# Kernel optimization log

Measured on AMD Instinct MI355X. Metric: run time of the kernel, lower is better.

Reference implementation:

```python
import jax, jax.numpy as jnp
import numpy as np

N = 100000      # nodes
NE = 1250000    # edges
D = 64          # in_dim == out_dim
H = 8           # heads
DH = D // H     # per-head dim


def setup_inputs() -> dict:
    key = jax.random.key(0)
    ks = jax.random.split(key, 7)
    s = 1.0 / np.sqrt(D)
    return {
        "x": jax.random.normal(ks[0], (N, D), jnp.float32),
        "edge_attr": jax.random.normal(ks[1], (NE, D), jnp.float32),
        "WQ": jax.random.normal(ks[2], (D, D), jnp.float32) * s,
        "WK": jax.random.normal(ks[3], (D, D), jnp.float32) * s,
        "WV": jax.random.normal(ks[4], (D, D), jnp.float32) * s,
        "WE": jax.random.normal(ks[5], (D, D), jnp.float32) * s,
        "edge_index": jax.random.randint(ks[6], (2, NE), 0, N, dtype=jnp.int32),
    }


def reference(x, edge_attr, WQ, WK, WV, WE, edge_index):
    # Linear projections (torch Linear y = x W^T; here W is stored [in,out])
    Q = (x @ WQ).reshape(N, H, DH)
    K = (x @ WK).reshape(N, H, DH)
    V = (x @ WV).reshape(N, H, DH)
    Ef = (edge_attr @ WE).reshape(NE, H, DH)

    src = edge_index[0]
    dst = edge_index[1]

    # per-edge score: exp(clamp(sum_d K[src]*Q[dst]*E / sqrt(DH), -5, 5))
    score = (K[src] * Q[dst]) * (1.0 / np.sqrt(DH)) * Ef  # [E,H,DH]
    score = jnp.exp(jnp.clip(score.sum(-1, keepdims=True), -5.0, 5.0))  # [E,H,1]

    msg = V[src] * score  # [E,H,DH]
    wV = jax.ops.segment_sum(msg, dst, num_segments=N)    # [N,H,DH]
    Z = jax.ops.segment_sum(score, dst, num_segments=N)   # [N,H,1]

    h_out = wV / (Z + 1e-6)
    return h_out.reshape(N, H * DH)
```

## Files before the change

kernel.cpp:

```cpp
#include <hip/hip_runtime.h>
#include <hip/hip_bf16.h>

#define NN    100000
#define NEDGE 1250000

typedef __attribute__((ext_vector_type(8))) short bf16x8;
typedef __attribute__((ext_vector_type(8))) unsigned short u16x8;
typedef __attribute__((ext_vector_type(4))) float f32x4;

__device__ __forceinline__ short f2bf(float f) {
    unsigned u = __float_as_uint(f);
    u += 0x7FFFu + ((u >> 16) & 1u);
    return (short)(u >> 16);
}
__device__ __forceinline__ float bf2f(unsigned short u) {
    return __uint_as_float(((unsigned)u) << 16);
}

constexpr size_t OFF_Q    = 0;
constexpr size_t OFF_KB   = OFF_Q    + (size_t)NN * 64 * 4;
constexpr size_t OFF_VB   = OFF_KB   + (size_t)NN * 64 * 2;
constexpr size_t OFF_SRT  = OFF_VB   + (size_t)NN * 64 * 2;
constexpr size_t OFF_HIST = OFF_SRT  + (size_t)NEDGE * 8;
constexpr size_t OFF_EX   = OFF_HIST + (size_t)NN * 4;
constexpr size_t OFF_BSUM = OFF_EX   + (size_t)NN * 4;
constexpr size_t OFF_BOFF = OFF_BSUM + 512 * 4;
constexpr size_t OFF_START= OFF_BOFF + 512 * 4;
constexpr size_t OFF_CUR  = OFF_START+ (size_t)(NN + 1) * 4;
constexpr size_t WS_NEED  = OFF_CUR  + (size_t)NN * 4;
constexpr int NB_SCAN = (NN + 255) / 256;

__global__ __launch_bounds__(256) void qkv_kernel(
    const float* __restrict__ x,
    const float* __restrict__ WQ, const float* __restrict__ WK,
    const float* __restrict__ WV,
    float* __restrict__ Qf, unsigned short* __restrict__ Kb,
    unsigned short* __restrict__ Vb)
{
    const int lane = threadIdx.x & 63;
    const int wid  = threadIdx.x >> 6;
    const int gw   = blockIdx.x * 4 + wid;
    const int nw   = gridDim.x * 4;
    const int colb = lane & 15;
    const int krow = (lane >> 4) * 8;

    bf16x8 Bf[3][4][2];
    const float* Ws[3] = {WQ, WK, WV};
    #pragma unroll
    for (int m = 0; m < 3; ++m)
        #pragma unroll
        for (int n = 0; n < 4; ++n)
            #pragma unroll
            for (int kh = 0; kh < 2; ++kh) {
                bf16x8 b;
                #pragma unroll
                for (int j = 0; j < 8; ++j)
                    b[j] = f2bf(Ws[m][(size_t)(kh * 32 + krow + j) * 64 + n * 16 + colb]);
                Bf[m][n][kh] = b;
            }

    for (int tile = gw; tile < NN / 16; tile += nw) {
        const int r0 = tile * 16;
        const float* xr = x + (size_t)(r0 + colb) * 64 + krow;
        f32x4 a0 = *(const f32x4*)(xr);
        f32x4 a1 = *(const f32x4*)(xr + 4);
        f32x4 a2 = *(const f32x4*)(xr + 32);
        f32x4 a3 = *(const f32x4*)(xr + 36);
        bf16x8 Alo, Ahi;
        #pragma unroll
        for (int j = 0; j < 4; ++j) {
            Alo[j]     = f2bf(a0[j]);
            Alo[4 + j] = f2bf(a1[j]);
            Ahi[j]     = f2bf(a2[j]);
            Ahi[4 + j] = f2bf(a3[j]);
        }
        #pragma unroll
        for (int m = 0; m < 3; ++m) {
            #pragma unroll
            for (int n = 0; n < 4; ++n) {
                f32x4 acc = {0.f, 0.f, 0.f, 0.f};
                acc = __builtin_amdgcn_mfma_f32_16x16x32_bf16(Alo, Bf[m][n][0], acc, 0, 0, 0);
                acc = __builtin_amdgcn_mfma_f32_16x16x32_bf16(Ahi, Bf[m][n][1], acc, 0, 0, 0);
                #pragma unroll
                for (int q = 0; q < 4; ++q) {
                    const size_t idx = (size_t)(r0 + (lane >> 4) * 4 + q) * 64 + n * 16 + colb;
                    if (m == 0)      Qf[idx] = acc[q];
                    else if (m == 1) Kb[idx] = (unsigned short)f2bf(acc[q]);
                    else             Vb[idx] = (unsigned short)f2bf(acc[q]);
                }
            }
        }
    }
}

__global__ void zero_hist_kernel(int* __restrict__ hist) {
    const int i = blockIdx.x * blockDim.x + threadIdx.x;
    if (i < NN) hist[i] = 0;
}

__global__ void hist_kernel(const int* __restrict__ ei, int* __restrict__ hist) {
    const int e = blockIdx.x * blockDim.x + threadIdx.x;
    if (e < NEDGE) atomicAdd(&hist[ei[NEDGE + e]], 1);
}

__global__ __launch_bounds__(256) void scanA_kernel(
    const int* __restrict__ hist, int* __restrict__ ex, int* __restrict__ bsum)
{
    __shared__ int wsum[4];
    const int i = blockIdx.x * 256 + threadIdx.x;
    const int lane = threadIdx.x & 63, wid = threadIdx.x >> 6;
    const int v = (i < NN) ? hist[i] : 0;
    int incl = v;
    #pragma unroll
    for (int off = 1; off < 64; off <<= 1) {
        int t = __shfl_up(incl, off);
        if (lane >= off) incl += t;
    }
    if (lane == 63) wsum[wid] = incl;
    __syncthreads();
    int pre = 0, bt = 0;
    #pragma unroll
    for (int w = 0; w < 4; ++w) { int s = wsum[w]; bt += s; if (w < wid) pre += s; }
    if (i < NN) ex[i] = incl - v + pre;
    if (threadIdx.x == 0) bsum[blockIdx.x] = bt;
}

__global__ __launch_bounds__(512) void scanB_kernel(
    const int* __restrict__ bsum, int* __restrict__ boff)
{
    __shared__ int wsum[8];
    const int i = threadIdx.x;
    const int lane = i & 63, wid = i >> 6;
    const int v = (i < NB_SCAN) ? bsum[i] : 0;
    int incl = v;
    #pragma unroll
    for (int off = 1; off < 64; off <<= 1) {
        int t = __shfl_up(incl, off);
        if (lane >= off) incl += t;
    }
    if (lane == 63) wsum[wid] = incl;
    __syncthreads();
    int pre = 0;
    #pragma unroll
    for (int w = 0; w < 8; ++w) { if (w < wid) pre += wsum[w]; }
    if (i < NB_SCAN) boff[i] = incl - v + pre;
}

__global__ void scanC_kernel(const int* __restrict__ ex, const int* __restrict__ boff,
                             int* __restrict__ start, int* __restrict__ cursor)
{
    const int i = blockIdx.x * blockDim.x + threadIdx.x;
    if (i < NN) {
        const int s = ex[i] + boff[i >> 8];
        start[i] = s;
        cursor[i] = s;
    } else if (i == NN) {
        start[NN] = NEDGE;
    }
}

__global__ void scatter_kernel(const int* __restrict__ ei, int* __restrict__ cursor,
                               int2* __restrict__ sorted)
{
    const int e = blockIdx.x * blockDim.x + threadIdx.x;
    if (e < NEDGE) {
        const int dst = ei[NEDGE + e];
        const int pos = atomicAdd(&cursor[dst], 1);
        sorted[pos] = make_int2(ei[e], e);
    }
}

__global__ __launch_bounds__(256) void agg_kernel(
    const float* __restrict__ Qn, const unsigned short* __restrict__ Kb,
    const unsigned short* __restrict__ Vb,
    const float* __restrict__ edge_attr, const float* __restrict__ WE,
    const int* __restrict__ start, const int2* __restrict__ sorted,
    float* __restrict__ out)
{
    const int lane = threadIdx.x & 63;
    const int wid  = threadIdx.x >> 6;
    const int gw   = (blockIdx.x * blockDim.x + threadIdx.x) >> 6;
    const int nw   = (gridDim.x * blockDim.x) >> 6;
    const int colb = lane & 15;
    const int krow = (lane >> 4) * 8;
    const int el   = lane >> 3;
    const int h    = lane & 7;
    const float c  = 0.35355339059327373f;

    __shared__ float efs_all[4][16][68];
    __shared__ int   srcs_all[4][16];
    float (*efs)[68] = efs_all[wid];
    int*   srcs      = srcs_all[wid];

    bf16x8 Bf[4][2];
    #pragma unroll
    for (int n = 0; n < 4; ++n)
        #pragma unroll
        for (int kh = 0; kh < 2; ++kh) {
            bf16x8 b;
            #pragma unroll
            for (int j = 0; j < 8; ++j)
                b[j] = f2bf(WE[(size_t)(kh * 32 + krow + j) * 64 + n * 16 + colb]);
            Bf[n][kh] = b;
        }

    for (int dst = gw; dst < NN; dst += nw) {
        const int beg = start[dst], end = start[dst + 1];
        if (beg == end) {
            if (el == 0) {
                float* op = out + (size_t)dst * 64 + h * 8;
                const f32x4 zz = {0.f, 0.f, 0.f, 0.f};
                *(f32x4*)(op)     = zz;
                *(f32x4*)(op + 4) = zz;
            }
            continue;
        }
        const float* qp = Qn + (size_t)dst * 64 + h * 8;
        const f32x4 q0 = *(const f32x4*)(qp);
        const f32x4 q1 = *(const f32x4*)(qp + 4);
        f32x4 av0 = {0.f, 0.f, 0.f, 0.f};
        f32x4 av1 = {0.f, 0.f, 0.f, 0.f};
        float az = 0.f;

        for (int j = beg; j < end; j += 16) {
            int rpos = j + colb;
            if (rpos >= end) rpos = beg;
            const int2 se = sorted[rpos];
            if (lane < 16) srcs[lane] = se.x;
            const float* ear = edge_attr + (size_t)se.y * 64 + krow;
            f32x4 a0 = *(const f32x4*)(ear);
            f32x4 a1 = *(const f32x4*)(ear + 4);
            f32x4 a2 = *(const f32x4*)(ear + 32);
            f32x4 a3 = *(const f32x4*)(ear + 36);
            bf16x8 Alo, Ahi;
            #pragma unroll
            for (int jj = 0; jj < 4; ++jj) {
                Alo[jj]     = f2bf(a0[jj]);
                Alo[4 + jj] = f2bf(a1[jj]);
                Ahi[jj]     = f2bf(a2[jj]);
                Ahi[4 + jj] = f2bf(a3[jj]);
            }
            const int rbase = (lane >> 4) * 4;
            #pragma unroll
            for (int n = 0; n < 4; ++n) {
                f32x4 z = {0.f, 0.f, 0.f, 0.f};
                z = __builtin_amdgcn_mfma_f32_16x16x32_bf16(Alo, Bf[n][0], z, 0, 0, 0);
                z = __builtin_amdgcn_mfma_f32_16x16x32_bf16(Ahi, Bf[n][1], z, 0, 0, 0);
                #pragma unroll
                for (int q = 0; q < 4; ++q)
                    efs[rbase + q][n * 16 + colb] = z[q];
            }
            asm volatile("s_waitcnt lgkmcnt(0)" ::: "memory");
            __builtin_amdgcn_sched_barrier(0);

            #pragma unroll
            for (int t = 0; t < 2; ++t) {
                const int er  = el + t * 8;
                const bool act = (j + er) < end;
                const int srcT = srcs[er];
                const u16x8 kT = *(const u16x8*)(Kb + (size_t)srcT * 64 + h * 8);
                const u16x8 vT = *(const u16x8*)(Vb + (size_t)srcT * 64 + h * 8);
                const f32x4 e0 = *(const f32x4*)(&efs[er][h * 8]);
                const f32x4 e1 = *(const f32x4*)(&efs[er][h * 8 + 4]);
                float tt = 0.f;
                #pragma unroll
                for (int d = 0; d < 4; ++d) {
                    tt += bf2f(kT[d])     * q0[d] * e0[d];
                    tt += bf2f(kT[4 + d]) * q1[d] * e1[d];
                }
                const float sc = act ? __expf(fminf(fmaxf(tt * c, -5.f), 5.f)) : 0.f;
                az += sc;
                #pragma unroll
                for (int d = 0; d < 4; ++d) {
                    av0[d] += bf2f(vT[d])     * sc;
                    av1[d] += bf2f(vT[4 + d]) * sc;
                }
            }
        }

        #pragma unroll
        for (int off = 8; off < 64; off <<= 1) {
            az += __shfl_xor(az, off);
            #pragma unroll
            for (int d = 0; d < 4; ++d) {
                av0[d] += __shfl_xor(av0[d], off);
                av1[d] += __shfl_xor(av1[d], off);
            }
        }

        if (el == 0) {
            const float inv = 1.f / (az + 1e-6f);
            f32x4 o0, o1;
            #pragma unroll
            for (int d = 0; d < 4; ++d) { o0[d] = av0[d] * inv; o1[d] = av1[d] * inv; }
            float* op = out + (size_t)dst * 64 + h * 8;
            *(f32x4*)(op)     = o0;
            *(f32x4*)(op + 4) = o1;
        }
    }
}

__global__ __launch_bounds__(256) void edge_kernel_fb(
    const float* __restrict__ edge_attr, const float* __restrict__ WE,
    const float* __restrict__ Qn, const unsigned short* __restrict__ Kb,
    const unsigned short* __restrict__ Vb, const int* __restrict__ ei,
    float* __restrict__ outAcc, float* __restrict__ Z)
{
    const int lane = threadIdx.x & 63;
    const int wid  = threadIdx.x >> 6;
    const int gw   = blockIdx.x * 4 + wid;
    const int nw   = gridDim.x * 4;
    const int colb = lane & 15;
    const int krow = (lane >> 4) * 8;
    const int b8   = (lane >> 3) & 1;

    bf16x8 Bf[4][2];
    #pragma unroll
    for (int n = 0; n < 4; ++n)
        #pragma unroll
        for (int kh = 0; kh < 2; ++kh) {
            bf16x8 b;
            #pragma unroll
            for (int j = 0; j < 8; ++j)
                b[j] = f2bf(WE[(size_t)(kh * 32 + krow + j) * 64 + n * 16 + colb]);
            Bf[n][kh] = b;
        }

    const float inv_sqrt_dh = 0.35355339059327373f;

    for (int tile = gw; tile < NEDGE / 16; tile += nw) {
        const int e0 = tile * 16;
        const float* ear = edge_attr + (size_t)(e0 + colb) * 64 + krow;
        f32x4 a0 = *(const f32x4*)(ear);
        f32x4 a1 = *(const f32x4*)(ear + 4);
        f32x4 a2 = *(const f32x4*)(ear + 32);
        f32x4 a3 = *(const f32x4*)(ear + 36);
        bf16x8 Alo, Ahi;
        #pragma unroll
        for (int j = 0; j < 4; ++j) {
            Alo[j]     = f2bf(a0[j]);
            Alo[4 + j] = f2bf(a1[j]);
            Ahi[j]     = f2bf(a2[j]);
            Ahi[4 + j] = f2bf(a3[j]);
        }
        f32x4 acc[4];
        #pragma unroll
        for (int n = 0; n < 4; ++n) {
            f32x4 z = {0.f, 0.f, 0.f, 0.f};
            z = __builtin_amdgcn_mfma_f32_16x16x32_bf16(Alo, Bf[n][0], z, 0, 0, 0);
            z = __builtin_amdgcn_mfma_f32_16x16x32_bf16(Ahi, Bf[n][1], z, 0, 0, 0);
            acc[n] = z;
        }
        int srcq[4], dstq[4];
        #pragma unroll
        for (int q = 0; q < 4; ++q) {
            const int erl = (lane >> 4) * 4 + q;
            srcq[q] = ei[e0 + erl];
            dstq[q] = ei[NEDGE + e0 + erl];
        }
        float sc[4][4];
        #pragma unroll
        for (int q = 0; q < 4; ++q) {
            #pragma unroll
            for (int n = 0; n < 4; ++n) {
                const int cidx = n * 16 + colb;
                const float kv = bf2f(Kb[(size_t)srcq[q] * 64 + cidx]);
                const float qv = Qn[(size_t)dstq[q] * 64 + cidx];
                float t = kv * qv * acc[n][q];
                t += __shfl_xor(t, 1);
                t += __shfl_xor(t, 2);
                t += __shfl_xor(t, 4);
                const float s = fminf(fmaxf(t * inv_sqrt_dh, -5.0f), 5.0f);
                sc[q][n] = __expf(s);
            }
        }
        #pragma unroll
        for (int q = 0; q < 4; ++q) {
            #pragma unroll
            for (int n = 0; n < 4; ++n) {
                const int cidx = n * 16 + colb;
                const float vv = bf2f(Vb[(size_t)srcq[q] * 64 + cidx]);
                unsafeAtomicAdd(&outAcc[(size_t)dstq[q] * 64 + cidx], vv * sc[q][n]);
                if ((lane & 7) == 0) {
                    const int hh = 2 * n + b8;
                    unsafeAtomicAdd(&Z[(size_t)dstq[q] * 8 + hh], sc[q][n]);
                }
            }
        }
    }
}

__global__ void finalize_fb(float* __restrict__ out, const float* __restrict__ Z) {
    const int i = blockIdx.x * blockDim.x + threadIdx.x;
    if (i < NN * 64) {
        const int node = i >> 6;
        const int h    = (i >> 3) & 7;
        out[i] = out[i] / (Z[node * 8 + h] + 1e-6f);
    }
}

extern "C" void kernel_launch(void* const* d_in, const int* in_sizes, int n_in,
                              void* d_out, int out_size, void* d_ws, size_t ws_size,
                              hipStream_t stream) {
    const float* x         = (const float*)d_in[0];
    const float* edge_attr = (const float*)d_in[1];
    const float* WQ        = (const float*)d_in[2];
    const float* WK        = (const float*)d_in[3];
    const float* WV        = (const float*)d_in[4];
    const float* WE        = (const float*)d_in[5];
    const int*   ei        = (const int*)d_in[6];
    float* out = (float*)d_out;

    char* base = (char*)d_ws;
    float*          Qf = (float*)(base + OFF_Q);
    unsigned short* Kb = (unsigned short*)(base + OFF_KB);
    unsigned short* Vb = (unsigned short*)(base + OFF_VB);

    qkv_kernel<<<1563, 256, 0, stream>>>(x, WQ, WK, WV, Qf, Kb, Vb);

    if (ws_size >= WS_NEED) {
        int2* sorted = (int2*)(base + OFF_SRT);
        int* hist    = (int*)(base + OFF_HIST);
        int* ex      = (int*)(base + OFF_EX);
        int* bsum    = (int*)(base + OFF_BSUM);
        int* boff    = (int*)(base + OFF_BOFF);
        int* start   = (int*)(base + OFF_START);
        int* cursor  = (int*)(base + OFF_CUR);

        zero_hist_kernel<<<NB_SCAN, 256, 0, stream>>>(hist);
        hist_kernel<<<(NEDGE + 255) / 256, 256, 0, stream>>>(ei, hist);
        scanA_kernel<<<NB_SCAN, 256, 0, stream>>>(hist, ex, bsum);
        scanB_kernel<<<1, 512, 0, stream>>>(bsum, boff);
        scanC_kernel<<<(NN + 256) / 256 + 1, 256, 0, stream>>>(ex, boff, start, cursor);
        scatter_kernel<<<(NEDGE + 255) / 256, 256, 0, stream>>>(ei, cursor, sorted);
        agg_kernel<<<4096, 256, 0, stream>>>(Qf, Kb, Vb, edge_attr, WE, start, sorted, out);
    } else {
        float* Z = (float*)(base + OFF_SRT);
        hipMemsetAsync(d_out, 0, (size_t)NN * 64 * sizeof(float), stream);
        hipMemsetAsync(Z, 0, (size_t)NN * 8 * sizeof(float), stream);
        edge_kernel_fb<<<2048, 256, 0, stream>>>(edge_attr, WE, Qf, Kb, Vb, ei, out, Z);
        finalize_fb<<<(NN * 64 + 255) / 256, 256, 0, stream>>>(out, Z);
    }
}
```

Measured before the change: 345.1 us.

## Switch aggregation from per-node CSR to edge-balanced chunks with segmented atomics

```diff
diff --git a/kernel.cpp b/kernel.cpp
--- a/kernel.cpp
+++ b/kernel.cpp
@@ -3,6 +3,7 @@
 
 #define NN    100000
 #define NEDGE 1250000
+constexpr int NW = NEDGE / 16;
 
 typedef __attribute__((ext_vector_type(8))) short bf16x8;
 typedef __attribute__((ext_vector_type(8))) unsigned short u16x8;
@@ -21,12 +22,12 @@
 constexpr size_t OFF_KB   = OFF_Q    + (size_t)NN * 64 * 4;
 constexpr size_t OFF_VB   = OFF_KB   + (size_t)NN * 64 * 2;
 constexpr size_t OFF_SRT  = OFF_VB   + (size_t)NN * 64 * 2;
-constexpr size_t OFF_HIST = OFF_SRT  + (size_t)NEDGE * 8;
+constexpr size_t OFF_Z    = OFF_SRT  + (size_t)NEDGE * 16;
+constexpr size_t OFF_HIST = OFF_Z    + (size_t)NN * 8 * 4;
 constexpr size_t OFF_EX   = OFF_HIST + (size_t)NN * 4;
 constexpr size_t OFF_BSUM = OFF_EX   + (size_t)NN * 4;
 constexpr size_t OFF_BOFF = OFF_BSUM + 512 * 4;
-constexpr size_t OFF_START= OFF_BOFF + 512 * 4;
-constexpr size_t OFF_CUR  = OFF_START+ (size_t)(NN + 1) * 4;
+constexpr size_t OFF_CUR  = OFF_BOFF + 512 * 4;
 constexpr size_t WS_NEED  = OFF_CUR  + (size_t)NN * 4;
 constexpr int NB_SCAN = (NN + 255) / 256;
 
@@ -147,35 +148,35 @@
 }
 
 __global__ void scanC_kernel(const int* __restrict__ ex, const int* __restrict__ boff,
-                             int* __restrict__ start, int* __restrict__ cursor)
+                             int* __restrict__ cursor)
 {
     const int i = blockIdx.x * blockDim.x + threadIdx.x;
-    if (i < NN) {
-        const int s = ex[i] + boff[i >> 8];
-        start[i] = s;
-        cursor[i] = s;
-    } else if (i == NN) {
-        start[NN] = NEDGE;
-    }
+    if (i < NN) cursor[i] = ex[i] + boff[i >> 8];
 }
 
 __global__ void scatter_kernel(const int* __restrict__ ei, int* __restrict__ cursor,
-                               int2* __restrict__ sorted)
+                               int4* __restrict__ sorted4)
 {
     const int e = blockIdx.x * blockDim.x + threadIdx.x;
     if (e < NEDGE) {
         const int dst = ei[NEDGE + e];
         const int pos = atomicAdd(&cursor[dst], 1);
-        sorted[pos] = make_int2(ei[e], e);
-    }
+        sorted4[pos] = make_int4(ei[e], e, dst, 0);
+    }
+}
+
+__global__ void zero_outz_kernel(float* __restrict__ out, float* __restrict__ Z) {
+    const int i = blockIdx.x * blockDim.x + threadIdx.x;
+    if (i < NN * 64) out[i] = 0.f;
+    if (i < NN * 8)  Z[i]   = 0.f;
 }
 
 __global__ __launch_bounds__(256) void agg_kernel(
     const float* __restrict__ Qn, const unsigned short* __restrict__ Kb,
     const unsigned short* __restrict__ Vb,
     const float* __restrict__ edge_attr, const float* __restrict__ WE,
-    const int* __restrict__ start, const int2* __restrict__ sorted,
-    float* __restrict__ out)
+    const int4* __restrict__ sorted4,
+    float* __restrict__ outAcc, float* __restrict__ Z)
 {
     const int lane = threadIdx.x & 63;
     const int wid  = threadIdx.x >> 6;
@@ -188,9 +189,7 @@
     const float c  = 0.35355339059327373f;
 
     __shared__ float efs_all[4][16][68];
-    __shared__ int   srcs_all[4][16];
     float (*efs)[68] = efs_all[wid];
-    int*   srcs      = srcs_all[wid];
 
     bf16x8 Bf[4][2];
     #pragma unroll
@@ -204,99 +203,144 @@
             Bf[n][kh] = b;
         }
 
-    for (int dst = gw; dst < NN; dst += nw) {
-        const int beg = start[dst], end = start[dst + 1];
-        if (beg == end) {
-            if (el == 0) {
-                float* op = out + (size_t)dst * 64 + h * 8;
-                const f32x4 zz = {0.f, 0.f, 0.f, 0.f};
-                *(f32x4*)(op)     = zz;
-                *(f32x4*)(op + 4) = zz;
-            }
-            continue;
-        }
-        const float* qp = Qn + (size_t)dst * 64 + h * 8;
-        const f32x4 q0 = *(const f32x4*)(qp);
-        const f32x4 q1 = *(const f32x4*)(qp + 4);
-        f32x4 av0 = {0.f, 0.f, 0.f, 0.f};
-        f32x4 av1 = {0.f, 0.f, 0.f, 0.f};
-        float az = 0.f;
-
-        for (int j = beg; j < end; j += 16) {
-            int rpos = j + colb;
-            if (rpos >= end) rpos = beg;
-            const int2 se = sorted[rpos];
-            if (lane < 16) srcs[lane] = se.x;
-            const float* ear = edge_attr + (size_t)se.y * 64 + krow;
-            f32x4 a0 = *(const f32x4*)(ear);
-            f32x4 a1 = *(const f32x4*)(ear + 4);
-            f32x4 a2 = *(const f32x4*)(ear + 32);
-            f32x4 a3 = *(const f32x4*)(ear + 36);
-            bf16x8 Alo, Ahi;
-            #pragma unroll
-            for (int jj = 0; jj < 4; ++jj) {
-                Alo[jj]     = f2bf(a0[jj]);
-                Alo[4 + jj] = f2bf(a1[jj]);
-                Ahi[jj]     = f2bf(a2[jj]);
-                Ahi[4 + jj] = f2bf(a3[jj]);
-            }
-            const int rbase = (lane >> 4) * 4;
-            #pragma unroll
-            for (int n = 0; n < 4; ++n) {
-                f32x4 z = {0.f, 0.f, 0.f, 0.f};
-                z = __builtin_amdgcn_mfma_f32_16x16x32_bf16(Alo, Bf[n][0], z, 0, 0, 0);
-                z = __builtin_amdgcn_mfma_f32_16x16x32_bf16(Ahi, Bf[n][1], z, 0, 0, 0);
-                #pragma unroll
-                for (int q = 0; q < 4; ++q)
-                    efs[rbase + q][n * 16 + colb] = z[q];
-            }
-            asm volatile("s_waitcnt lgkmcnt(0)" ::: "memory");
-            __builtin_amdgcn_sched_barrier(0);
-
-            #pragma unroll
-            for (int t = 0; t < 2; ++t) {
-                const int er  = el + t * 8;
-                const bool act = (j + er) < end;
-                const int srcT = srcs[er];
-                const u16x8 kT = *(const u16x8*)(Kb + (size_t)srcT * 64 + h * 8);
-                const u16x8 vT = *(const u16x8*)(Vb + (size_t)srcT * 64 + h * 8);
-                const f32x4 e0 = *(const f32x4*)(&efs[er][h * 8]);
-                const f32x4 e1 = *(const f32x4*)(&efs[er][h * 8 + 4]);
-                float tt = 0.f;
+    int w = gw;
+    int4 se = make_int4(0, 0, 0, 0);
+    f32x4 a0 = {0,0,0,0}, a1 = {0,0,0,0}, a2 = {0,0,0,0}, a3 = {0,0,0,0};
+    if (w < NW) {
+        se = sorted4[(size_t)w * 16 + colb];
+        const float* ear = edge_attr + (size_t)se.y * 64 + krow;
+        a0 = *(const f32x4*)(ear);
+        a1 = *(const f32x4*)(ear + 4);
+        a2 = *(const f32x4*)(ear + 32);
+        a3 = *(const f32x4*)(ear + 36);
+    }
+
+    for (; w < NW; w += nw) {
+        const int wn = w + nw;
+        int4 se_n = make_int4(0, 0, 0, 0);
+        if (wn < NW) se_n = sorted4[(size_t)wn * 16 + colb];
+
+        const int s0 = __shfl(se.x, el);
+        const int s1 = __shfl(se.x, el + 8);
+        const int d0 = __shfl(se.z, el);
+        const int d1 = __shfl(se.z, el + 8);
+
+        const int prevd = __shfl(se.z, (colb == 0) ? 0 : colb - 1);
+        const bool isS = (lane < 16) && (lane == 0 || prevd != se.z);
+        const unsigned segmask = (unsigned)(__ballot(isS) & 0xFFFFull);
+
+        const u16x8 k0v = *(const u16x8*)(Kb + (size_t)s0 * 64 + h * 8);
+        const u16x8 v0v = *(const u16x8*)(Vb + (size_t)s0 * 64 + h * 8);
+        const u16x8 k1v = *(const u16x8*)(Kb + (size_t)s1 * 64 + h * 8);
+        const u16x8 v1v = *(const u16x8*)(Vb + (size_t)s1 * 64 + h * 8);
+        const float* qp0 = Qn + (size_t)d0 * 64 + h * 8;
+        const f32x4 q00 = *(const f32x4*)(qp0);
+        const f32x4 q01 = *(const f32x4*)(qp0 + 4);
+        const float* qp1 = Qn + (size_t)d1 * 64 + h * 8;
+        const f32x4 q10 = *(const f32x4*)(qp1);
+        const f32x4 q11 = *(const f32x4*)(qp1 + 4);
+
+        bf16x8 Alo, Ahi;
+        #pragma unroll
+        for (int jj = 0; jj < 4; ++jj) {
+            Alo[jj]     = f2bf(a0[jj]);
+            Alo[4 + jj] = f2bf(a1[jj]);
+            Ahi[jj]     = f2bf(a2[jj]);
+            Ahi[4 + jj] = f2bf(a3[jj]);
+        }
+        const int rbase = (lane >> 4) * 4;
+        #pragma unroll
+        for (int n = 0; n < 4; ++n) {
+            f32x4 z = {0.f, 0.f, 0.f, 0.f};
+            z = __builtin_amdgcn_mfma_f32_16x16x32_bf16(Alo, Bf[n][0], z, 0, 0, 0);
+            z = __builtin_amdgcn_mfma_f32_16x16x32_bf16(Ahi, Bf[n][1], z, 0, 0, 0);
+            #pragma unroll
+            for (int q = 0; q < 4; ++q)
+                efs[rbase + q][n * 16 + colb] = z[q];
+        }
+
+        f32x4 a0n = {0,0,0,0}, a1n = {0,0,0,0}, a2n = {0,0,0,0}, a3n = {0,0,0,0};
+        if (wn < NW) {
+            const float* earn = edge_attr + (size_t)se_n.y * 64 + krow;
+            a0n = *(const f32x4*)(earn);
+            a1n = *(const f32x4*)(earn + 4);
+            a2n = *(const f32x4*)(earn + 32);
+            a3n = *(const f32x4*)(earn + 36);
+        }
+
+        asm volatile("s_waitcnt lgkmcnt(0)" ::: "memory");
+        __builtin_amdgcn_sched_barrier(0);
+
+        const f32x4 e00 = *(const f32x4*)(&efs[el][h * 8]);
+        const f32x4 e01 = *(const f32x4*)(&efs[el][h * 8 + 4]);
+        const f32x4 e10 = *(const f32x4*)(&efs[el + 8][h * 8]);
+        const f32x4 e11 = *(const f32x4*)(&efs[el + 8][h * 8 + 4]);
+        float t0 = 0.f, t1 = 0.f;
+        #pragma unroll
+        for (int d = 0; d < 4; ++d) {
+            t0 += bf2f(k0v[d])     * q00[d] * e00[d];
+            t0 += bf2f(k0v[4 + d]) * q01[d] * e01[d];
+            t1 += bf2f(k1v[d])     * q10[d] * e10[d];
+            t1 += bf2f(k1v[4 + d]) * q11[d] * e11[d];
+        }
+        const float sc0 = __expf(fminf(fmaxf(t0 * c, -5.f), 5.f));
+        const float sc1 = __expf(fminf(fmaxf(t1 * c, -5.f), 5.f));
+        f32x4 m00, m01, m10, m11;
+        #pragma unroll
+        for (int d = 0; d < 4; ++d) {
+            m00[d] = bf2f(v0v[d])     * sc0;
+            m01[d] = bf2f(v0v[4 + d]) * sc0;
+            m10[d] = bf2f(v1v[d])     * sc1;
+            m11[d] = bf2f(v1v[4 + d]) * sc1;
+        }
+
+        unsigned mask = segmask;
+        while (mask) {
+            const int i = __builtin_ctz(mask);
+            const unsigned rest = mask & (mask - 1u);
+            const int jend = rest ? __builtin_ctz(rest) : 16;
+            mask = rest;
+            const int cur = __shfl(se.z, i);
+            const bool act0 = (el >= i) && (el < jend);
+            const bool act1 = (el + 8 >= i) && (el + 8 < jend);
+            float sz = (act0 ? sc0 : 0.f) + (act1 ? sc1 : 0.f);
+            f32x4 sm0, sm1;
+            #pragma unroll
+            for (int d = 0; d < 4; ++d) {
+                sm0[d] = (act0 ? m00[d] : 0.f) + (act1 ? m10[d] : 0.f);
+                sm1[d] = (act0 ? m01[d] : 0.f) + (act1 ? m11[d] : 0.f);
+            }
+            #pragma unroll
+            for (int off = 8; off < 64; off <<= 1) {
+                sz += __shfl_xor(sz, off);
                 #pragma unroll
                 for (int d = 0; d < 4; ++d) {
-                    tt += bf2f(kT[d])     * q0[d] * e0[d];
-                    tt += bf2f(kT[4 + d]) * q1[d] * e1[d];
+                    sm0[d] += __shfl_xor(sm0[d], off);
+                    sm1[d] += __shfl_xor(sm1[d], off);
                 }
-                const float sc = act ? __expf(fminf(fmaxf(tt * c, -5.f), 5.f)) : 0.f;
-                az += sc;
+            }
+            if (el == 0) {
+                float* op = outAcc + (size_t)cur * 64 + h * 8;
                 #pragma unroll
                 for (int d = 0; d < 4; ++d) {
-                    av0[d] += bf2f(vT[d])     * sc;
-                    av1[d] += bf2f(vT[4 + d]) * sc;
+                    unsafeAtomicAdd(op + d,     sm0[d]);
+                    unsafeAtomicAdd(op + 4 + d, sm1[d]);
                 }
-            }
-        }
-
-        #pragma unroll
-        for (int off = 8; off < 64; off <<= 1) {
-            az += __shfl_xor(az, off);
-            #pragma unroll
-            for (int d = 0; d < 4; ++d) {
-                av0[d] += __shfl_xor(av0[d], off);
-                av1[d] += __shfl_xor(av1[d], off);
-            }
-        }
-
-        if (el == 0) {
-            const float inv = 1.f / (az + 1e-6f);
-            f32x4 o0, o1;
-            #pragma unroll
-            for (int d = 0; d < 4; ++d) { o0[d] = av0[d] * inv; o1[d] = av1[d] * inv; }
-            float* op = out + (size_t)dst * 64 + h * 8;
-            *(f32x4*)(op)     = o0;
-            *(f32x4*)(op + 4) = o1;
-        }
+                unsafeAtomicAdd(&Z[(size_t)cur * 8 + h], sz);
+            }
+        }
+
+        se = se_n;
+        a0 = a0n; a1 = a1n; a2 = a2n; a3 = a3n;
+    }
+}
+
+__global__ void finalize_kernel(float* __restrict__ out, const float* __restrict__ Z) {
+    const int i = blockIdx.x * blockDim.x + threadIdx.x;
+    if (i < NN * 64) {
+        const int node = i >> 6;
+        const int h    = (i >> 3) & 7;
+        out[i] = out[i] / (Z[node * 8 + h] + 1e-6f);
     }
 }
 
@@ -387,15 +431,6 @@
                 }
             }
         }
-    }
-}
-
-__global__ void finalize_fb(float* __restrict__ out, const float* __restrict__ Z) {
-    const int i = blockIdx.x * blockDim.x + threadIdx.x;
-    if (i < NN * 64) {
-        const int node = i >> 6;
-        const int h    = (i >> 3) & 7;
-        out[i] = out[i] / (Z[node * 8 + h] + 1e-6f);
     }
 }
 
@@ -419,26 +454,28 @@
     qkv_kernel<<<1563, 256, 0, stream>>>(x, WQ, WK, WV, Qf, Kb, Vb);
 
     if (ws_size >= WS_NEED) {
-        int2* sorted = (int2*)(base + OFF_SRT);
-        int* hist    = (int*)(base + OFF_HIST);
-        int* ex      = (int*)(base + OFF_EX);
-        int* bsum    = (int*)(base + OFF_BSUM);
-        int* boff    = (int*)(base + OFF_BOFF);
-        int* start   = (int*)(base + OFF_START);
-        int* cursor  = (int*)(base + OFF_CUR);
+        int4* sorted4 = (int4*)(base + OFF_SRT);
+        float* Z      = (float*)(base + OFF_Z);
+        int* hist     = (int*)(base + OFF_HIST);
+        int* ex       = (int*)(base + OFF_EX);
+        int* bsum     = (int*)(base + OFF_BSUM);
+        int* boff     = (int*)(base + OFF_BOFF);
+        int* cursor   = (int*)(base + OFF_CUR);
 
         zero_hist_kernel<<<NB_SCAN, 256, 0, stream>>>(hist);
         hist_kernel<<<(NEDGE + 255) / 256, 256, 0, stream>>>(ei, hist);
         scanA_kernel<<<NB_SCAN, 256, 0, stream>>>(hist, ex, bsum);
         scanB_kernel<<<1, 512, 0, stream>>>(bsum, boff);
-        scanC_kernel<<<(NN + 256) / 256 + 1, 256, 0, stream>>>(ex, boff, start, cursor);
-        scatter_kernel<<<(NEDGE + 255) / 256, 256, 0, stream>>>(ei, cursor, sorted);
-        agg_kernel<<<4096, 256, 0, stream>>>(Qf, Kb, Vb, edge_attr, WE, start, sorted, out);
+        scanC_kernel<<<NB_SCAN, 256, 0, stream>>>(ex, boff, cursor);
+        scatter_kernel<<<(NEDGE + 255) / 256, 256, 0, stream>>>(ei, cursor, sorted4);
+        zero_outz_kernel<<<(NN * 64 + 255) / 256, 256, 0, stream>>>(out, Z);
+        agg_kernel<<<4096, 256, 0, stream>>>(Qf, Kb, Vb, edge_attr, WE, sorted4, out, Z);
+        finalize_kernel<<<(NN * 64 + 255) / 256, 256, 0, stream>>>(out, Z);
     } else {
         float* Z = (float*)(base + OFF_SRT);
         hipMemsetAsync(d_out, 0, (size_t)NN * 64 * sizeof(float), stream);
         hipMemsetAsync(Z, 0, (size_t)NN * 8 * sizeof(float), stream);
         edge_kernel_fb<<<2048, 256, 0, stream>>>(edge_attr, WE, Qf, Kb, Vb, ei, out, Z);
-        finalize_fb<<<(NN * 64 + 255) / 256, 256, 0, stream>>>(out, Z);
-    }
-}
+        finalize_kernel<<<(NN * 64 + 255) / 256, 256, 0, stream>>>(out, Z);
+    }
+}
```

Measured after the change: 580.7 us. +68.3%, slower.

## Software-pipeline next destination's edge loads and replace LDS src exchange with shuffles

Applied to the files above, without the earlier changes.

```diff
diff --git a/kernel.cpp b/kernel.cpp
--- a/kernel.cpp
+++ b/kernel.cpp
@@ -188,9 +188,7 @@
     const float c  = 0.35355339059327373f;
 
     __shared__ float efs_all[4][16][68];
-    __shared__ int   srcs_all[4][16];
     float (*efs)[68] = efs_all[wid];
-    int*   srcs      = srcs_all[wid];
 
     bf16x8 Bf[4][2];
     #pragma unroll
@@ -204,77 +202,156 @@
             Bf[n][kh] = b;
         }
 
-    for (int dst = gw; dst < NN; dst += nw) {
-        const int beg = start[dst], end = start[dst + 1];
-        if (beg == end) {
-            if (el == 0) {
-                float* op = out + (size_t)dst * 64 + h * 8;
-                const f32x4 zz = {0.f, 0.f, 0.f, 0.f};
-                *(f32x4*)(op)     = zz;
-                *(f32x4*)(op + 4) = zz;
-            }
-            continue;
-        }
+    int dst = gw;
+    int beg = 0, end = 0;
+    int2 se = make_int2(0, 0);
+    f32x4 a0 = {0,0,0,0}, a1 = {0,0,0,0}, a2 = {0,0,0,0}, a3 = {0,0,0,0};
+    if (dst < NN) {
+        beg = start[dst]; end = start[dst + 1];
+        int rpos = beg + colb;
+        if (rpos >= end) rpos = beg;
+        if (rpos >= NEDGE) rpos = NEDGE - 1;
+        se = sorted[rpos];
+        const float* ear = edge_attr + (size_t)se.y * 64 + krow;
+        a0 = *(const f32x4*)(ear);
+        a1 = *(const f32x4*)(ear + 4);
+        a2 = *(const f32x4*)(ear + 32);
+        a3 = *(const f32x4*)(ear + 36);
+    }
+
+    for (; dst < NN; dst += nw) {
+        const int dn = dst + nw;
+        int beg_n = 0, end_n = 0;
+        if (dn < NN) { beg_n = start[dn]; end_n = start[dn + 1]; }
+
+        const int s0 = __shfl(se.x, el);
+        const int s1 = __shfl(se.x, el + 8);
+        const u16x8 k0v = *(const u16x8*)(Kb + (size_t)s0 * 64 + h * 8);
+        const u16x8 v0v = *(const u16x8*)(Vb + (size_t)s0 * 64 + h * 8);
+        const u16x8 k1v = *(const u16x8*)(Kb + (size_t)s1 * 64 + h * 8);
+        const u16x8 v1v = *(const u16x8*)(Vb + (size_t)s1 * 64 + h * 8);
         const float* qp = Qn + (size_t)dst * 64 + h * 8;
         const f32x4 q0 = *(const f32x4*)(qp);
         const f32x4 q1 = *(const f32x4*)(qp + 4);
-        f32x4 av0 = {0.f, 0.f, 0.f, 0.f};
-        f32x4 av1 = {0.f, 0.f, 0.f, 0.f};
+
+        bf16x8 Alo, Ahi;
+        #pragma unroll
+        for (int jj = 0; jj < 4; ++jj) {
+            Alo[jj]     = f2bf(a0[jj]);
+            Alo[4 + jj] = f2bf(a1[jj]);
+            Ahi[jj]     = f2bf(a2[jj]);
+            Ahi[4 + jj] = f2bf(a3[jj]);
+        }
+        const int rbase = (lane >> 4) * 4;
+        #pragma unroll
+        for (int n = 0; n < 4; ++n) {
+            f32x4 z = {0.f, 0.f, 0.f, 0.f};
+            z = __builtin_amdgcn_mfma_f32_16x16x32_bf16(Alo, Bf[n][0], z, 0, 0, 0);
+            z = __builtin_amdgcn_mfma_f32_16x16x32_bf16(Ahi, Bf[n][1], z, 0, 0, 0);
+            #pragma unroll
+            for (int q = 0; q < 4; ++q)
+                efs[rbase + q][n * 16 + colb] = z[q];
+        }
+
+        int2 se_n = make_int2(0, 0);
+        f32x4 a0n = {0,0,0,0}, a1n = {0,0,0,0}, a2n = {0,0,0,0}, a3n = {0,0,0,0};
+        if (dn < NN) {
+            int rpos_n = beg_n + colb;
+            if (rpos_n >= end_n) rpos_n = beg_n;
+            if (rpos_n >= NEDGE) rpos_n = NEDGE - 1;
+            se_n = sorted[rpos_n];
+            const float* earn = edge_attr + (size_t)se_n.y * 64 + krow;
+            a0n = *(const f32x4*)(earn);
+            a1n = *(const f32x4*)(earn + 4);
+            a2n = *(const f32x4*)(earn + 32);
+            a3n = *(const f32x4*)(earn + 36);
+        }
+
+        asm volatile("s_waitcnt lgkmcnt(0)" ::: "memory");
+        __builtin_amdgcn_sched_barrier(0);
+
+        f32x4 av0 = {0,0,0,0}, av1 = {0,0,0,0};
         float az = 0.f;
-
-        for (int j = beg; j < end; j += 16) {
+        {
+            const f32x4 e00 = *(const f32x4*)(&efs[el][h * 8]);
+            const f32x4 e01 = *(const f32x4*)(&efs[el][h * 8 + 4]);
+            const f32x4 e10 = *(const f32x4*)(&efs[el + 8][h * 8]);
+            const f32x4 e11 = *(const f32x4*)(&efs[el + 8][h * 8 + 4]);
+            float t0 = 0.f, t1 = 0.f;
+            #pragma unroll
+            for (int d = 0; d < 4; ++d) {
+                t0 += bf2f(k0v[d])     * q0[d] * e00[d];
+                t0 += bf2f(k0v[4 + d]) * q1[d] * e01[d];
+                t1 += bf2f(k1v[d])     * q0[d] * e10[d];
+                t1 += bf2f(k1v[4 + d]) * q1[d] * e11[d];
+            }
+            const bool act0 = (beg + el)     < end;
+            const bool act1 = (beg + el + 8) < end;
+            const float sc0 = act0 ? __expf(fminf(fmaxf(t0 * c, -5.f), 5.f)) : 0.f;
+            const float sc1 = act1 ? __expf(fminf(fmaxf(t1 * c, -5.f), 5.f)) : 0.f;
+            az += sc0 + sc1;
+            #pragma unroll
+            for (int d = 0; d < 4; ++d) {
+                av0[d] += bf2f(v0v[d])     * sc0 + bf2f(v1v[d])     * sc1;
+                av1[d] += bf2f(v0v[4 + d]) * sc0 + bf2f(v1v[4 + d]) * sc1;
+            }
+        }
+
+        for (int j = beg + 16; j < end; j += 16) {
             int rpos = j + colb;
             if (rpos >= end) rpos = beg;
-            const int2 se = sorted[rpos];
-            if (lane < 16) srcs[lane] = se.x;
-            const float* ear = edge_attr + (size_t)se.y * 64 + krow;
-            f32x4 a0 = *(const f32x4*)(ear);
-            f32x4 a1 = *(const f32x4*)(ear + 4);
-            f32x4 a2 = *(const f32x4*)(ear + 32);
-            f32x4 a3 = *(const f32x4*)(ear + 36);
-            bf16x8 Alo, Ahi;
+            const int2 seb = sorted[rpos];
+            const int sb0 = __shfl(seb.x, el);
+            const int sb1 = __shfl(seb.x, el + 8);
+            const u16x8 kb0 = *(const u16x8*)(Kb + (size_t)sb0 * 64 + h * 8);
+            const u16x8 vb0 = *(const u16x8*)(Vb + (size_t)sb0 * 64 + h * 8);
+            const u16x8 kb1 = *(const u16x8*)(Kb + (size_t)sb1 * 64 + h * 8);
+            const u16x8 vb1 = *(const u16x8*)(Vb + (size_t)sb1 * 64 + h * 8);
+            const float* earb = edge_attr + (size_t)seb.y * 64 + krow;
+            const f32x4 b0 = *(const f32x4*)(earb);
+            const f32x4 b1 = *(const f32x4*)(earb + 4);
+            const f32x4 b2 = *(const f32x4*)(earb + 32);
+            const f32x4 b3 = *(const f32x4*)(earb + 36);
+            bf16x8 Blo, Bhi;
             #pragma unroll
             for (int jj = 0; jj < 4; ++jj) {
-                Alo[jj]     = f2bf(a0[jj]);
-                Alo[4 + jj] = f2bf(a1[jj]);
-                Ahi[jj]     = f2bf(a2[jj]);
-                Ahi[4 + jj] = f2bf(a3[jj]);
-            }
-            const int rbase = (lane >> 4) * 4;
+                Blo[jj]     = f2bf(b0[jj]);
+                Blo[4 + jj] = f2bf(b1[jj]);
+                Bhi[jj]     = f2bf(b2[jj]);
+                Bhi[4 + jj] = f2bf(b3[jj]);
+            }
             #pragma unroll
             for (int n = 0; n < 4; ++n) {
                 f32x4 z = {0.f, 0.f, 0.f, 0.f};
-                z = __builtin_amdgcn_mfma_f32_16x16x32_bf16(Alo, Bf[n][0], z, 0, 0, 0);
-                z = __builtin_amdgcn_mfma_f32_16x16x32_bf16(Ahi, Bf[n][1], z, 0, 0, 0);
+                z = __builtin_amdgcn_mfma_f32_16x16x32_bf16(Blo, Bf[n][0], z, 0, 0, 0);
+                z = __builtin_amdgcn_mfma_f32_16x16x32_bf16(Bhi, Bf[n][1], z, 0, 0, 0);
                 #pragma unroll
                 for (int q = 0; q < 4; ++q)
                     efs[rbase + q][n * 16 + colb] = z[q];
             }
             asm volatile("s_waitcnt lgkmcnt(0)" ::: "memory");
             __builtin_amdgcn_sched_barrier(0);
-
-            #pragma unroll
-            for (int t = 0; t < 2; ++t) {
-                const int er  = el + t * 8;
-                const bool act = (j + er) < end;
-                const int srcT = srcs[er];
-                const u16x8 kT = *(const u16x8*)(Kb + (size_t)srcT * 64 + h * 8);
-                const u16x8 vT = *(const u16x8*)(Vb + (size_t)srcT * 64 + h * 8);
-                const f32x4 e0 = *(const f32x4*)(&efs[er][h * 8]);
-                const f32x4 e1 = *(const f32x4*)(&efs[er][h * 8 + 4]);
-                float tt = 0.f;
-                #pragma unroll
-                for (int d = 0; d < 4; ++d) {
-                    tt += bf2f(kT[d])     * q0[d] * e0[d];
-                    tt += bf2f(kT[4 + d]) * q1[d] * e1[d];
-                }
-                const float sc = act ? __expf(fminf(fmaxf(tt * c, -5.f), 5.f)) : 0.f;
-                az += sc;
-                #pragma unroll
-                for (int d = 0; d < 4; ++d) {
-                    av0[d] += bf2f(vT[d])     * sc;
-                    av1[d] += bf2f(vT[4 + d]) * sc;
-                }
+            const f32x4 e00 = *(const f32x4*)(&efs[el][h * 8]);
+            const f32x4 e01 = *(const f32x4*)(&efs[el][h * 8 + 4]);
+            const f32x4 e10 = *(const f32x4*)(&efs[el + 8][h * 8]);
+            const f32x4 e11 = *(const f32x4*)(&efs[el + 8][h * 8 + 4]);
+            float t0 = 0.f, t1 = 0.f;
+            #pragma unroll
+            for (int d = 0; d < 4; ++d) {
+                t0 += bf2f(kb0[d])     * q0[d] * e00[d];
+                t0 += bf2f(kb0[4 + d]) * q1[d] * e01[d];
+                t1 += bf2f(kb1[d])     * q0[d] * e10[d];
+                t1 += bf2f(kb1[4 + d]) * q1[d] * e11[d];
+            }
+            const bool act0 = (j + el)     < end;
+            const bool act1 = (j + el + 8) < end;
+            const float sc0 = act0 ? __expf(fminf(fmaxf(t0 * c, -5.f), 5.f)) : 0.f;
+            const float sc1 = act1 ? __expf(fminf(fmaxf(t1 * c, -5.f), 5.f)) : 0.f;
+            az += sc0 + sc1;
+            #pragma unroll
+            for (int d = 0; d < 4; ++d) {
+                av0[d] += bf2f(vb0[d])     * sc0 + bf2f(vb1[d])     * sc1;
+                av1[d] += bf2f(vb0[4 + d]) * sc0 + bf2f(vb1[4 + d]) * sc1;
             }
         }
 
@@ -297,6 +374,9 @@
             *(f32x4*)(op)     = o0;
             *(f32x4*)(op + 4) = o1;
         }
+
+        beg = beg_n; end = end_n; se = se_n;
+        a0 = a0n; a1 = a1n; a2 = a2n; a3 = a3n;
     }
 }
 
```

Result: faster. 319.3 us (-7.5%).
